# Kernel tuning notes

Hardware: AMD Instinct MI355X
Metric: run time of the kernel (lower is better)

The kernel has to match this reference:

```python
import jax, jax.numpy as jnp
import numpy as np

D = 1024      # n_embd
H = 16        # n_head
DH = D // H   # head dim = 64
FF = 4 * D    # 4096
EPS = 1e-5
MASKED_BIAS = -10000.0


def gelu_new(x):
    # GPT-2 'gelu_new': 0.5*x*(1+tanh(sqrt(2/pi)*(x+0.044715*x^3)))
    c = np.sqrt(2.0 / np.pi).astype(np.float32)
    return 0.5 * x * (1.0 + jnp.tanh(c * (x + 0.044715 * x * x * x)))


def layer_norm(x, g, b):
    mu = jnp.mean(x, axis=-1, keepdims=True)
    var = jnp.mean(jnp.square(x - mu), axis=-1, keepdims=True)
    return (x - mu) * jax.lax.rsqrt(var + EPS) * g + b


def setup_inputs() -> dict:
    key = jax.random.key(0)
    ks = jax.random.split(key, 8)
    B, S = 4, 2048
    std = 0.02
    return {
        "hidden_states": jax.random.normal(ks[0], (B, S, D), jnp.float32),
        "ln1_g": jnp.ones((D,), jnp.float32),
        "ln1_b": jnp.zeros((D,), jnp.float32),
        "w_attn": std * jax.random.normal(ks[1], (D, 3 * D), jnp.float32),
        "b_attn": jnp.zeros((3 * D,), jnp.float32),
        "w_attn_proj": std * jax.random.normal(ks[2], (D, D), jnp.float32),
        "b_attn_proj": jnp.zeros((D,), jnp.float32),
        "ln2_g": jnp.ones((D,), jnp.float32),
        "ln2_b": jnp.zeros((D,), jnp.float32),
        "w_fc": std * jax.random.normal(ks[3], (D, FF), jnp.float32),
        "b_fc": jnp.zeros((FF,), jnp.float32),
        "w_mlp_proj": std * jax.random.normal(ks[4], (FF, D), jnp.float32),
        "b_mlp_proj": jnp.zeros((D,), jnp.float32),
    }


def reference(hidden_states, ln1_g, ln1_b, w_attn, b_attn, w_attn_proj, b_attn_proj,
              ln2_g, ln2_b, w_fc, b_fc, w_mlp_proj, b_mlp_proj):
    B, S, _ = hidden_states.shape

    # --- self-attention ---
    x = layer_norm(hidden_states, ln1_g, ln1_b)
    qkv = x @ w_attn + b_attn                       # [B,S,3D]
    q, k, v = jnp.split(qkv, 3, axis=-1)
    # split heads -> [B,H,S,DH]
    q = q.reshape(B, S, H, DH).transpose(0, 2, 1, 3)
    k = k.reshape(B, S, H, DH).transpose(0, 2, 1, 3)
    v = v.reshape(B, S, H, DH).transpose(0, 2, 1, 3)

    w = jnp.einsum('bhqd,bhkd->bhqk', q, k) / jnp.sqrt(jnp.float32(DH))
    causal = jnp.tril(jnp.ones((S, S), bool))       # [S,S]
    w = jnp.where(causal, w, jnp.float32(MASKED_BIAS))
    w = jax.nn.softmax(w, axis=-1)
    a = jnp.einsum('bhqk,bhkd->bhqd', w, v)         # [B,H,S,DH]
    a = a.transpose(0, 2, 1, 3).reshape(B, S, D)
    a = a @ w_attn_proj + b_attn_proj
    hidden_states = hidden_states + a

    # --- MLP ---
    m = layer_norm(hidden_states, ln2_g, ln2_b)
    m = gelu_new(m @ w_fc + b_fc) @ w_mlp_proj + b_mlp_proj
    return hidden_states + m
```

## Files before the change

kernel.cpp:

```cpp
#include <hip/hip_runtime.h>
#include <hip/hip_bf16.h>
#include <cstddef>

#define SEQ   2048
#define DMODEL 1024
#define NHEAD 16
#define HDIM  64
#define FFDIM 4096

typedef __attribute__((ext_vector_type(8))) short bf16x8;
typedef __attribute__((ext_vector_type(4))) short bf16x4;
typedef __attribute__((ext_vector_type(4))) float f32x4;

__device__ __forceinline__ unsigned short f2b(float x) {
  __hip_bfloat16 h = __float2bfloat16(x);
  return __builtin_bit_cast(unsigned short, h);
}
__device__ __forceinline__ float b2f(short u) {
  unsigned x = ((unsigned)(unsigned short)u) << 16;
  return __builtin_bit_cast(float, x);
}
__device__ __forceinline__ void gl16(const short* g, short* l) {
  __builtin_amdgcn_global_load_lds(
      (const __attribute__((address_space(1))) void*)g,
      (__attribute__((address_space(3))) void*)l, 16, 0, 0);
}

__global__ __launch_bounds__(256)
void ln_kernel(const float* __restrict__ x, const float* __restrict__ g,
               const float* __restrict__ b, short* __restrict__ y) {
  const int row = blockIdx.x;
  const int t = threadIdx.x;
  const float* xr = x + (size_t)row * DMODEL;
  float4 v = *(const float4*)(xr + t * 4);
  float s = v.x + v.y + v.z + v.w;
  float q = v.x * v.x + v.y * v.y + v.z * v.z + v.w * v.w;
  #pragma unroll
  for (int off = 32; off; off >>= 1) {
    s += __shfl_xor(s, off);
    q += __shfl_xor(q, off);
  }
  __shared__ float ss[4], qq[4];
  if ((t & 63) == 0) { ss[t >> 6] = s; qq[t >> 6] = q; }
  __syncthreads();
  s = ss[0] + ss[1] + ss[2] + ss[3];
  q = qq[0] + qq[1] + qq[2] + qq[3];
  const float mean = s * (1.f / DMODEL);
  const float var = q * (1.f / DMODEL) - mean * mean;
  const float rstd = rsqrtf(var + 1e-5f);
  float4 gv = *(const float4*)(g + t * 4);
  float4 bv = *(const float4*)(b + t * 4);
  bf16x4 o;
  o[0] = (short)f2b((v.x - mean) * rstd * gv.x + bv.x);
  o[1] = (short)f2b((v.y - mean) * rstd * gv.y + bv.y);
  o[2] = (short)f2b((v.z - mean) * rstd * gv.z + bv.z);
  o[3] = (short)f2b((v.w - mean) * rstd * gv.w + bv.w);
  *(bf16x4*)(y + (size_t)row * DMODEL + t * 4) = o;
}

__device__ __forceinline__ float gelu_new_f(float x) {
  const float c = 0.7978845608028654f;
  float u = c * (x + 0.044715f * x * x * x);
  float e = __expf(2.f * u);
  float t = 1.f - 2.f / (e + 1.f);
  return 0.5f * x * (1.f + t);
}

__global__ __launch_bounds__(256)
void wconv_kernel(const float* __restrict__ W, short* __restrict__ Wt,
                  int K, int N) {
  const int n0 = blockIdx.x * 64, k0 = blockIdx.y * 64;
  const int t = threadIdx.x;
  __shared__ short tile[64][72];
  #pragma unroll
  for (int i = 0; i < 4; ++i) {
    const int row = i * 16 + (t >> 4);
    const int col4 = (t & 15) * 4;
    float4 v = *(const float4*)(W + (size_t)(k0 + row) * N + n0 + col4);
    tile[col4 + 0][row] = (short)f2b(v.x);
    tile[col4 + 1][row] = (short)f2b(v.y);
    tile[col4 + 2][row] = (short)f2b(v.z);
    tile[col4 + 3][row] = (short)f2b(v.w);
  }
  __syncthreads();
  #pragma unroll
  for (int i = 0; i < 2; ++i) {
    const int cc = t + i * 256;
    const int nr = cc >> 3, k8 = (cc & 7) * 8;
    bf16x8 vv;
    #pragma unroll
    for (int j = 0; j < 8; ++j) vv[j] = tile[nr][k8 + j];
    *(bf16x8*)(Wt + (size_t)(n0 + nr) * K + k0 + k8) = vv;
  }
}

template <bool OUTBF, bool GELU, bool RES>
__global__ __launch_bounds__(256)
void gemm_bf16(const short* __restrict__ A, const short* __restrict__ Bt,
               const float* __restrict__ bias, const float* __restrict__ R,
               void* __restrict__ C, int M, int N, int K) {
  __shared__ short As[128 * 64];
  __shared__ short Bs[128 * 64];
  const int t = threadIdx.x, lane = t & 63, w = t >> 6;
  const int g = lane >> 4, la = lane & 15;
  const int bn = blockIdx.x, bm = blockIdx.y;
  const int wm = w >> 1, wn = w & 1;

  const int srow = t >> 3;
  const int scolb = ((t & 7) * 16) ^ ((srow & 7) << 4);
  const short* Ag = A + (size_t)(bm * 128 + srow) * K + (scolb >> 1);
  const short* Bg = Bt + (size_t)(bn * 128 + srow) * K + (scolb >> 1);
  short* Asl = As + t * 8;
  short* Bsl = Bs + t * 8;

  f32x4 acc[4][4];
  #pragma unroll
  for (int i = 0; i < 4; ++i)
    #pragma unroll
    for (int j = 0; j < 4; ++j) acc[i][j] = (f32x4){0.f, 0.f, 0.f, 0.f};

  const int KT = K >> 6;
  for (int kt = 0; kt < KT; ++kt) {
    __syncthreads();
    #pragma unroll
    for (int i = 0; i < 4; ++i) {
      gl16(Ag + (size_t)i * 32 * K + kt * 64, Asl + i * 2048);
      gl16(Bg + (size_t)i * 32 * K + kt * 64, Bsl + i * 2048);
    }
    __syncthreads();
    #pragma unroll
    for (int ks = 0; ks < 2; ++ks) {
      bf16x8 af[4], bfr[4];
      #pragma unroll
      for (int mi = 0; mi < 4; ++mi) {
        const int row = wm * 64 + mi * 16 + la;
        af[mi] = *(const bf16x8*)((const char*)As + row * 128 +
                                  ((ks * 64 + g * 16) ^ ((row & 7) << 4)));
      }
      #pragma unroll
      for (int ni = 0; ni < 4; ++ni) {
        const int row = wn * 64 + ni * 16 + la;
        bfr[ni] = *(const bf16x8*)((const char*)Bs + row * 128 +
                                   ((ks * 64 + g * 16) ^ ((row & 7) << 4)));
      }
      #pragma unroll
      for (int mi = 0; mi < 4; ++mi)
        #pragma unroll
        for (int ni = 0; ni < 4; ++ni)
          acc[mi][ni] = __builtin_amdgcn_mfma_f32_16x16x32_bf16(
              af[mi], bfr[ni], acc[mi][ni], 0, 0, 0);
    }
  }

  const int crow0 = bm * 128 + wm * 64 + g * 4;
  const int ccol0 = bn * 128 + wn * 64 + la;
  float bl[4];
  #pragma unroll
  for (int ni = 0; ni < 4; ++ni) bl[ni] = bias[ccol0 + ni * 16];
  #pragma unroll
  for (int mi = 0; mi < 4; ++mi) {
    #pragma unroll
    for (int r = 0; r < 4; ++r) {
      const size_t row = (size_t)(crow0 + mi * 16 + r);
      #pragma unroll
      for (int ni = 0; ni < 4; ++ni) {
        float v = acc[mi][ni][r] + bl[ni];
        if (GELU) v = gelu_new_f(v);
        if (RES) v += R[row * N + ccol0 + ni * 16];
        if (OUTBF)
          ((short*)C)[row * N + ccol0 + ni * 16] = (short)f2b(v);
        else
          ((float*)C)[row * N + ccol0 + ni * 16] = v;
      }
    }
  }
}

__global__ __launch_bounds__(256)
void prep_kernel(const short* __restrict__ qkv, short* __restrict__ Qb,
                 short* __restrict__ Kb, short* __restrict__ Vtb) {
  const int st = blockIdx.x, h = blockIdx.y, b = blockIdx.z;
  const int t = threadIdx.x;
  const int s0 = st * 64;
  const size_t bh = (size_t)b * NHEAD + h;
  __shared__ short vt[64][72];
  #pragma unroll
  for (int i = 0; i < 2; ++i) {
    const int cc = t + i * 256;
    const int r = cc >> 3, d8 = (cc & 7) * 8;
    const short* src = qkv + ((size_t)b * SEQ + s0 + r) * 3072 + h * 64 + d8;
    bf16x8 q8 = *(const bf16x8*)(src);
    #pragma unroll
    for (int j = 0; j < 8; ++j) q8[j] = (short)f2b(b2f(q8[j]) * 0.125f);
    *(bf16x8*)(Qb + (bh * SEQ + s0 + r) * 64 + d8) = q8;
    bf16x8 k8 = *(const bf16x8*)(src + 1024);
    *(bf16x8*)(Kb + (bh * SEQ + s0 + r) * 64 + d8) = k8;
    bf16x8 v8 = *(const bf16x8*)(src + 2048);
    #pragma unroll
    for (int j = 0; j < 8; ++j) vt[d8 + j][r] = v8[j];
  }
  __syncthreads();
  #pragma unroll
  for (int i = 0; i < 2; ++i) {
    const int cc = t + i * 256;
    const int d = cc >> 3, s8 = (cc & 7) * 8;
    bf16x8 vv;
    #pragma unroll
    for (int j = 0; j < 8; ++j) vv[j] = vt[d][s8 + j];
    *(bf16x8*)(Vtb + (bh * 64 + d) * SEQ + s0 + s8) = vv;
  }
}

__global__ __launch_bounds__(256)
void mha_kernel(const short* __restrict__ Qb, const short* __restrict__ Kb,
                const short* __restrict__ Vtb, short* __restrict__ out) {
  const int qt = blockIdx.x, h = blockIdx.y, b = blockIdx.z;
  const int t = threadIdx.x, lane = t & 63, w = t >> 6;
  const int g = lane >> 4, la = lane & 15;
  const size_t bh = (size_t)b * NHEAD + h;

  __shared__ short Ks[64 * 64];
  __shared__ short Vts[64 * 64];
  __shared__ short Ps[4][16 * 64];

  const short* qrow = Qb + (bh * SEQ + (size_t)qt * 64 + w * 16 + la) * 64;
  const bf16x8 qf0 = *(const bf16x8*)(qrow + g * 8);
  const bf16x8 qf1 = *(const bf16x8*)(qrow + 32 + g * 8);

  float o[16];
  #pragma unroll
  for (int i = 0; i < 16; ++i) o[i] = 0.f;
  float m = -1e30f, l = 0.f;

  const int sr0 = t >> 3, sc8 = (t & 7) * 8;

  for (int kt = 0; kt <= qt; ++kt) {
    const int k0 = kt * 64;
    __syncthreads();
    #pragma unroll
    for (int i = 0; i < 2; ++i) {
      const int r = sr0 + i * 32;
      bf16x8 kv = *(const bf16x8*)(Kb + (bh * SEQ + k0 + r) * 64 + sc8);
      bf16x8 vv = *(const bf16x8*)(Vtb + (bh * 64 + r) * SEQ + k0 + sc8);
      const int lb = r * 128 + ((sc8 * 2) ^ ((r & 7) << 4));
      *(bf16x8*)((char*)Ks + lb) = kv;
      *(bf16x8*)((char*)Vts + lb) = vv;
    }
    __syncthreads();

    float sv[16];
    #pragma unroll
    for (int mt = 0; mt < 4; ++mt) {
      const int ar = mt * 16 + la;
      const int ab = ar * 128 + ((g * 16) ^ ((ar & 7) << 4));
      bf16x8 ka0 = *(const bf16x8*)((char*)Ks + ab);
      bf16x8 ka1 = *(const bf16x8*)((char*)Ks + (ab ^ 64));
      f32x4 sa = {0.f, 0.f, 0.f, 0.f};
      sa = __builtin_amdgcn_mfma_f32_16x16x32_bf16(ka0, qf0, sa, 0, 0, 0);
      sa = __builtin_amdgcn_mfma_f32_16x16x32_bf16(ka1, qf1, sa, 0, 0, 0);
      sv[mt * 4 + 0] = sa[0]; sv[mt * 4 + 1] = sa[1];
      sv[mt * 4 + 2] = sa[2]; sv[mt * 4 + 3] = sa[3];
    }

    if (kt == qt) {
      const int qrel = w * 16 + la;
      #pragma unroll
      for (int idx = 0; idx < 16; ++idx) {
        const int krel = (idx >> 2) * 16 + g * 4 + (idx & 3);
        if (krel > qrel) sv[idx] = -10000.0f;
      }
    }

    float tmax = sv[0];
    #pragma unroll
    for (int i = 1; i < 16; ++i) tmax = fmaxf(tmax, sv[i]);
    tmax = fmaxf(tmax, __shfl_xor(tmax, 16));
    tmax = fmaxf(tmax, __shfl_xor(tmax, 32));
    const float mn = fmaxf(m, tmax);
    const float sc = __expf(m - mn);
    m = mn;
    float ps = 0.f;
    #pragma unroll
    for (int i = 0; i < 16; ++i) { sv[i] = __expf(sv[i] - mn); ps += sv[i]; }
    ps += __shfl_xor(ps, 16);
    ps += __shfl_xor(ps, 32);
    l = l * sc + ps;
    #pragma unroll
    for (int r = 0; r < 4; ++r) {
      const float scr = __shfl(sc, (g << 2) + r);
      o[r] *= scr; o[4 + r] *= scr; o[8 + r] *= scr; o[12 + r] *= scr;
    }
    #pragma unroll
    for (int mt = 0; mt < 4; ++mt) {
      #pragma unroll
      for (int r2 = 0; r2 < 2; ++r2) {
        const unsigned pk = (unsigned)f2b(sv[mt * 4 + r2 * 2]) |
                            ((unsigned)f2b(sv[mt * 4 + r2 * 2 + 1]) << 16);
        const int kk = mt * 16 + g * 4 + r2 * 2;
        const int pb = la * 128 + ((kk * 2) ^ ((la & 7) << 4));
        *(unsigned*)((char*)Ps[w] + pb) = pk;
      }
    }
    asm volatile("s_waitcnt lgkmcnt(0)" ::: "memory");
    __builtin_amdgcn_sched_barrier(0);

    const int pb0 = la * 128 + ((g * 16) ^ ((la & 7) << 4));
    const bf16x8 pa0 = *(const bf16x8*)((char*)Ps[w] + pb0);
    const bf16x8 pa1 = *(const bf16x8*)((char*)Ps[w] + (pb0 ^ 64));
    #pragma unroll
    for (int nt = 0; nt < 4; ++nt) {
      const int dr = nt * 16 + la;
      const int vb = dr * 128 + ((g * 16) ^ ((dr & 7) << 4));
      bf16x8 vb0 = *(const bf16x8*)((char*)Vts + vb);
      bf16x8 vb1 = *(const bf16x8*)((char*)Vts + (vb ^ 64));
      f32x4 oa = {o[nt * 4 + 0], o[nt * 4 + 1], o[nt * 4 + 2], o[nt * 4 + 3]};
      oa = __builtin_amdgcn_mfma_f32_16x16x32_bf16(pa0, vb0, oa, 0, 0, 0);
      oa = __builtin_amdgcn_mfma_f32_16x16x32_bf16(pa1, vb1, oa, 0, 0, 0);
      o[nt * 4 + 0] = oa[0]; o[nt * 4 + 1] = oa[1];
      o[nt * 4 + 2] = oa[2]; o[nt * 4 + 3] = oa[3];
    }
  }

  const float linv = 1.f / l;
  #pragma unroll
  for (int r = 0; r < 4; ++r) {
    const float li = __shfl(linv, (g << 2) + r);
    const int qrow_g = qt * 64 + w * 16 + g * 4 + r;
    #pragma unroll
    for (int nt = 0; nt < 4; ++nt) {
      out[((size_t)b * SEQ + qrow_g) * DMODEL + h * 64 + nt * 16 + la] =
          (short)f2b(o[nt * 4 + r] * li);
    }
  }
}

extern "C" void kernel_launch(void* const* d_in, const int* in_sizes, int n_in,
                              void* d_out, int out_size, void* d_ws, size_t ws_size,
                              hipStream_t stream) {
  const float* hidden      = (const float*)d_in[0];
  const float* ln1_g       = (const float*)d_in[1];
  const float* ln1_b       = (const float*)d_in[2];
  const float* w_attn      = (const float*)d_in[3];
  const float* b_attn      = (const float*)d_in[4];
  const float* w_attn_proj = (const float*)d_in[5];
  const float* b_attn_proj = (const float*)d_in[6];
  const float* ln2_g       = (const float*)d_in[7];
  const float* ln2_b       = (const float*)d_in[8];
  const float* w_fc        = (const float*)d_in[9];
  const float* b_fc        = (const float*)d_in[10];
  const float* w_mlp_proj  = (const float*)d_in[11];
  const float* b_mlp_proj  = (const float*)d_in[12];
  float* out = (float*)d_out;

  const int Bn = in_sizes[0] / (SEQ * DMODEL);
  const int M = Bn * SEQ;

  char* W = (char*)d_ws;
  const size_t szMD2 = (size_t)M * DMODEL * 2;
  short* xln_b  = (short*)W;
  short* qkv_b  = (short*)(W + szMD2);
  short* a1_b   = qkv_b;
  char*  p2     = W + szMD2 + (size_t)M * FFDIM * 2;
  short* Qb     = (short*)p2;
  short* Kb     = Qb + (size_t)M * DMODEL;
  short* Vtb    = Kb + (size_t)M * DMODEL;
  short* attn_b = Vtb + (size_t)M * DMODEL;
  float* h2     = (float*)(p2 + 4 * szMD2);
  short* wat    = (short*)(p2 + 4 * szMD2 + (size_t)M * DMODEL * 4);
  short* wpt    = wat + (size_t)3 * DMODEL * DMODEL;
  short* wft    = wpt + (size_t)DMODEL * DMODEL;
  short* wmt    = wft + (size_t)FFDIM * DMODEL;

  wconv_kernel<<<dim3(3 * DMODEL / 64, DMODEL / 64), 256, 0, stream>>>(
      w_attn, wat, DMODEL, 3 * DMODEL);
  wconv_kernel<<<dim3(DMODEL / 64, DMODEL / 64), 256, 0, stream>>>(
      w_attn_proj, wpt, DMODEL, DMODEL);
  wconv_kernel<<<dim3(FFDIM / 64, DMODEL / 64), 256, 0, stream>>>(
      w_fc, wft, DMODEL, FFDIM);
  wconv_kernel<<<dim3(DMODEL / 64, FFDIM / 64), 256, 0, stream>>>(
      w_mlp_proj, wmt, FFDIM, DMODEL);

  ln_kernel<<<M, 256, 0, stream>>>(hidden, ln1_g, ln1_b, xln_b);
  gemm_bf16<true, false, false><<<dim3(3 * DMODEL / 128, M / 128), 256, 0, stream>>>(
      xln_b, wat, b_attn, nullptr, qkv_b, M, 3 * DMODEL, DMODEL);
  prep_kernel<<<dim3(SEQ / 64, NHEAD, Bn), 256, 0, stream>>>(qkv_b, Qb, Kb, Vtb);
  mha_kernel<<<dim3(SEQ / 64, NHEAD, Bn), 256, 0, stream>>>(Qb, Kb, Vtb, attn_b);
  gemm_bf16<false, false, true><<<dim3(DMODEL / 128, M / 128), 256, 0, stream>>>(
      attn_b, wpt, b_attn_proj, hidden, h2, M, DMODEL, DMODEL);
  ln_kernel<<<M, 256, 0, stream>>>(h2, ln2_g, ln2_b, xln_b);
  gemm_bf16<true, true, false><<<dim3(FFDIM / 128, M / 128), 256, 0, stream>>>(
      xln_b, wft, b_fc, nullptr, a1_b, M, FFDIM, DMODEL);
  gemm_bf16<false, false, true><<<dim3(DMODEL / 128, M / 128), 256, 0, stream>>>(
      a1_b, wmt, b_mlp_proj, h2, out, M, DMODEL, FFDIM);
}
```

Before: 618.6 us.

## Pair causal query tiles per block and streamline flash-attention softmax

The attention kernel now processes two query tiles per block (p and QT-1-p), so every block does about the same causal work, and it launches half as many blocks. Softmax switches to exp2, with log2(e) folded into the Q scale and the mask constant. A lazy rescale skips the output correction when the running max grows by little, and the max and sum reductions become trees. K/V tiles are loaded with direct global-to-LDS loads, and the four weight-conversion launches are merged into one. The lazy-rescale threshold lets unnormalized values grow up to 2^11.5 before correction, which carries a small numerical risk.

```diff
diff --git a/kernel.cpp b/kernel.cpp
--- a/kernel.cpp
+++ b/kernel.cpp
@@ -7,6 +7,7 @@
 #define NHEAD 16
 #define HDIM  64
 #define FFDIM 4096
+#define QT    (SEQ / 64)
 
 typedef __attribute__((ext_vector_type(8))) short bf16x8;
 typedef __attribute__((ext_vector_type(4))) short bf16x4;
@@ -67,9 +68,18 @@
 }
 
 __global__ __launch_bounds__(256)
-void wconv_kernel(const float* __restrict__ W, short* __restrict__ Wt,
-                  int K, int N) {
-  const int n0 = blockIdx.x * 64, k0 = blockIdx.y * 64;
+void wconv4_kernel(const float* __restrict__ w0, short* __restrict__ t0,
+                   const float* __restrict__ w1, short* __restrict__ t1,
+                   const float* __restrict__ w2, short* __restrict__ t2,
+                   const float* __restrict__ w3, short* __restrict__ t3) {
+  int id = blockIdx.x;
+  const float* W; short* Wt; int K, N;
+  if (id < 768)       { W = w0; Wt = t0; K = 1024; N = 3072; }
+  else if (id < 1024) { id -= 768;  W = w1; Wt = t1; K = 1024; N = 1024; }
+  else if (id < 2048) { id -= 1024; W = w2; Wt = t2; K = 1024; N = 4096; }
+  else                { id -= 2048; W = w3; Wt = t3; K = 4096; N = 1024; }
+  const int nt = N >> 6;
+  const int n0 = (id % nt) * 64, k0 = (id / nt) * 64;
   const int t = threadIdx.x;
   __shared__ short tile[64][72];
   #pragma unroll
@@ -183,6 +193,7 @@
   const int t = threadIdx.x;
   const int s0 = st * 64;
   const size_t bh = (size_t)b * NHEAD + h;
+  const float qscale = 0.125f * 1.44269504088896f;
   __shared__ short vt[64][72];
   #pragma unroll
   for (int i = 0; i < 2; ++i) {
@@ -191,7 +202,7 @@
     const short* src = qkv + ((size_t)b * SEQ + s0 + r) * 3072 + h * 64 + d8;
     bf16x8 q8 = *(const bf16x8*)(src);
     #pragma unroll
-    for (int j = 0; j < 8; ++j) q8[j] = (short)f2b(b2f(q8[j]) * 0.125f);
+    for (int j = 0; j < 8; ++j) q8[j] = (short)f2b(b2f(q8[j]) * qscale);
     *(bf16x8*)(Qb + (bh * SEQ + s0 + r) * 64 + d8) = q8;
     bf16x8 k8 = *(const bf16x8*)(src + 1024);
     *(bf16x8*)(Kb + (bh * SEQ + s0 + r) * 64 + d8) = k8;
@@ -214,7 +225,7 @@
 __global__ __launch_bounds__(256)
 void mha_kernel(const short* __restrict__ Qb, const short* __restrict__ Kb,
                 const short* __restrict__ Vtb, short* __restrict__ out) {
-  const int qt = blockIdx.x, h = blockIdx.y, b = blockIdx.z;
+  const int p = blockIdx.x, h = blockIdx.y, b = blockIdx.z;
   const int t = threadIdx.x, lane = t & 63, w = t >> 6;
   const int g = lane >> 4, la = lane & 15;
   const size_t bh = (size_t)b * NHEAD + h;
@@ -223,113 +234,134 @@
   __shared__ short Vts[64 * 64];
   __shared__ short Ps[4][16 * 64];
 
-  const short* qrow = Qb + (bh * SEQ + (size_t)qt * 64 + w * 16 + la) * 64;
-  const bf16x8 qf0 = *(const bf16x8*)(qrow + g * 8);
-  const bf16x8 qf1 = *(const bf16x8*)(qrow + 32 + g * 8);
-
-  float o[16];
-  #pragma unroll
-  for (int i = 0; i < 16; ++i) o[i] = 0.f;
-  float m = -1e30f, l = 0.f;
-
-  const int sr0 = t >> 3, sc8 = (t & 7) * 8;
-
-  for (int kt = 0; kt <= qt; ++kt) {
-    const int k0 = kt * 64;
-    __syncthreads();
-    #pragma unroll
-    for (int i = 0; i < 2; ++i) {
-      const int r = sr0 + i * 32;
-      bf16x8 kv = *(const bf16x8*)(Kb + (bh * SEQ + k0 + r) * 64 + sc8);
-      bf16x8 vv = *(const bf16x8*)(Vtb + (bh * 64 + r) * SEQ + k0 + sc8);
-      const int lb = r * 128 + ((sc8 * 2) ^ ((r & 7) << 4));
-      *(bf16x8*)((char*)Ks + lb) = kv;
-      *(bf16x8*)((char*)Vts + lb) = vv;
+  const int srow = t >> 3;
+  const int scolb = ((t & 7) * 16) ^ ((srow & 7) << 4);
+
+  #pragma unroll 1
+  for (int e = 0; e < 2; ++e) {
+    const int qt = e ? (QT - 1 - p) : p;
+
+    const short* qrow = Qb + (bh * SEQ + (size_t)qt * 64 + w * 16 + la) * 64;
+    const bf16x8 qf0 = *(const bf16x8*)(qrow + g * 8);
+    const bf16x8 qf1 = *(const bf16x8*)(qrow + 32 + g * 8);
+
+    float o[16];
+    #pragma unroll
+    for (int i = 0; i < 16; ++i) o[i] = 0.f;
+    float m = -1e30f, l = 0.f;
+
+    for (int kt = 0; kt <= qt; ++kt) {
+      const int k0 = kt * 64;
+      __syncthreads();
+      #pragma unroll
+      for (int i = 0; i < 2; ++i) {
+        const int r = srow + i * 32;
+        gl16(Kb + (bh * SEQ + k0 + r) * 64 + (scolb >> 1), Ks + i * 2048 + t * 8);
+        gl16(Vtb + (bh * 64 + r) * SEQ + k0 + (scolb >> 1), Vts + i * 2048 + t * 8);
+      }
+      __syncthreads();
+
+      float sv[16];
+      #pragma unroll
+      for (int mt = 0; mt < 4; ++mt) {
+        const int ar = mt * 16 + la;
+        const int ab = ar * 128 + ((g * 16) ^ ((ar & 7) << 4));
+        bf16x8 ka0 = *(const bf16x8*)((char*)Ks + ab);
+        bf16x8 ka1 = *(const bf16x8*)((char*)Ks + (ab ^ 64));
+        f32x4 sa = {0.f, 0.f, 0.f, 0.f};
+        sa = __builtin_amdgcn_mfma_f32_16x16x32_bf16(ka0, qf0, sa, 0, 0, 0);
+        sa = __builtin_amdgcn_mfma_f32_16x16x32_bf16(ka1, qf1, sa, 0, 0, 0);
+        sv[mt * 4 + 0] = sa[0]; sv[mt * 4 + 1] = sa[1];
+        sv[mt * 4 + 2] = sa[2]; sv[mt * 4 + 3] = sa[3];
+      }
+
+      if (kt == qt) {
+        const int qrel = w * 16 + la;
+        #pragma unroll
+        for (int idx = 0; idx < 16; ++idx) {
+          const int krel = (idx >> 2) * 16 + g * 4 + (idx & 3);
+          if (krel > qrel) sv[idx] = -14426.950408889634f;
+        }
+      }
+
+      float t8[8], t4[4], t2[2];
+      #pragma unroll
+      for (int i = 0; i < 8; ++i) t8[i] = fmaxf(sv[2 * i], sv[2 * i + 1]);
+      #pragma unroll
+      for (int i = 0; i < 4; ++i) t4[i] = fmaxf(t8[2 * i], t8[2 * i + 1]);
+      t2[0] = fmaxf(t4[0], t4[1]); t2[1] = fmaxf(t4[2], t4[3]);
+      float tmax = fmaxf(t2[0], t2[1]);
+      tmax = fmaxf(tmax, __shfl_xor(tmax, 16));
+      tmax = fmaxf(tmax, __shfl_xor(tmax, 32));
+
+      const bool skip = __all(tmax <= m + 11.5f) != 0;
+      const float mn = skip ? m : fmaxf(m, tmax);
+
+      float ss8[8], ss4[4];
+      #pragma unroll
+      for (int i = 0; i < 16; ++i) sv[i] = exp2f(sv[i] - mn);
+      #pragma unroll
+      for (int i = 0; i < 8; ++i) ss8[i] = sv[2 * i] + sv[2 * i + 1];
+      #pragma unroll
+      for (int i = 0; i < 4; ++i) ss4[i] = ss8[2 * i] + ss8[2 * i + 1];
+      float ps = (ss4[0] + ss4[1]) + (ss4[2] + ss4[3]);
+      ps += __shfl_xor(ps, 16);
+      ps += __shfl_xor(ps, 32);
+
+      if (skip) {
+        l += ps;
+      } else {
+        const float sc = exp2f(m - mn);
+        l = l * sc + ps;
+        m = mn;
+        #pragma unroll
+        for (int r = 0; r < 4; ++r) {
+          const float scr = __shfl(sc, (g << 2) + r);
+          o[r] *= scr; o[4 + r] *= scr; o[8 + r] *= scr; o[12 + r] *= scr;
+        }
+      }
+
+      #pragma unroll
+      for (int mt = 0; mt < 4; ++mt) {
+        #pragma unroll
+        for (int r2 = 0; r2 < 2; ++r2) {
+          const unsigned pk = (unsigned)f2b(sv[mt * 4 + r2 * 2]) |
+                              ((unsigned)f2b(sv[mt * 4 + r2 * 2 + 1]) << 16);
+          const int kk = mt * 16 + g * 4 + r2 * 2;
+          const int pb = la * 128 + ((kk * 2) ^ ((la & 7) << 4));
+          *(unsigned*)((char*)Ps[w] + pb) = pk;
+        }
+      }
+      asm volatile("s_waitcnt lgkmcnt(0)" ::: "memory");
+      __builtin_amdgcn_sched_barrier(0);
+
+      const int pb0 = la * 128 + ((g * 16) ^ ((la & 7) << 4));
+      const bf16x8 pa0 = *(const bf16x8*)((char*)Ps[w] + pb0);
+      const bf16x8 pa1 = *(const bf16x8*)((char*)Ps[w] + (pb0 ^ 64));
+      #pragma unroll
+      for (int nt = 0; nt < 4; ++nt) {
+        const int dr = nt * 16 + la;
+        const int vb = dr * 128 + ((g * 16) ^ ((dr & 7) << 4));
+        bf16x8 vb0 = *(const bf16x8*)((char*)Vts + vb);
+        bf16x8 vb1 = *(const bf16x8*)((char*)Vts + (vb ^ 64));
+        f32x4 oa = {o[nt * 4 + 0], o[nt * 4 + 1], o[nt * 4 + 2], o[nt * 4 + 3]};
+        oa = __builtin_amdgcn_mfma_f32_16x16x32_bf16(pa0, vb0, oa, 0, 0, 0);
+        oa = __builtin_amdgcn_mfma_f32_16x16x32_bf16(pa1, vb1, oa, 0, 0, 0);
+        o[nt * 4 + 0] = oa[0]; o[nt * 4 + 1] = oa[1];
+        o[nt * 4 + 2] = oa[2]; o[nt * 4 + 3] = oa[3];
+      }
     }
-    __syncthreads();
-
-    float sv[16];
-    #pragma unroll
-    for (int mt = 0; mt < 4; ++mt) {
-      const int ar = mt * 16 + la;
-      const int ab = ar * 128 + ((g * 16) ^ ((ar & 7) << 4));
-      bf16x8 ka0 = *(const bf16x8*)((char*)Ks + ab);
-      bf16x8 ka1 = *(const bf16x8*)((char*)Ks + (ab ^ 64));
-      f32x4 sa = {0.f, 0.f, 0.f, 0.f};
-      sa = __builtin_amdgcn_mfma_f32_16x16x32_bf16(ka0, qf0, sa, 0, 0, 0);
-      sa = __builtin_amdgcn_mfma_f32_16x16x32_bf16(ka1, qf1, sa, 0, 0, 0);
-      sv[mt * 4 + 0] = sa[0]; sv[mt * 4 + 1] = sa[1];
-      sv[mt * 4 + 2] = sa[2]; sv[mt * 4 + 3] = sa[3];
-    }
-
-    if (kt == qt) {
-      const int qrel = w * 16 + la;
-      #pragma unroll
-      for (int idx = 0; idx < 16; ++idx) {
-        const int krel = (idx >> 2) * 16 + g * 4 + (idx & 3);
-        if (krel > qrel) sv[idx] = -10000.0f;
-      }
-    }
-
-    float tmax = sv[0];
-    #pragma unroll
-    for (int i = 1; i < 16; ++i) tmax = fmaxf(tmax, sv[i]);
-    tmax = fmaxf(tmax, __shfl_xor(tmax, 16));
-    tmax = fmaxf(tmax, __shfl_xor(tmax, 32));
-    const float mn = fmaxf(m, tmax);
-    const float sc = __expf(m - mn);
-    m = mn;
-    float ps = 0.f;
-    #pragma unroll
-    for (int i = 0; i < 16; ++i) { sv[i] = __expf(sv[i] - mn); ps += sv[i]; }
-    ps += __shfl_xor(ps, 16);
-    ps += __shfl_xor(ps, 32);
-    l = l * sc + ps;
+
+    const float linv = 1.f / l;
     #pragma unroll
     for (int r = 0; r < 4; ++r) {
-      const float scr = __shfl(sc, (g << 2) + r);
-      o[r] *= scr; o[4 + r] *= scr; o[8 + r] *= scr; o[12 + r] *= scr;
-    }
-    #pragma unroll
-    for (int mt = 0; mt < 4; ++mt) {
-      #pragma unroll
-      for (int r2 = 0; r2 < 2; ++r2) {
-        const unsigned pk = (unsigned)f2b(sv[mt * 4 + r2 * 2]) |
-                            ((unsigned)f2b(sv[mt * 4 + r2 * 2 + 1]) << 16);
-        const int kk = mt * 16 + g * 4 + r2 * 2;
-        const int pb = la * 128 + ((kk * 2) ^ ((la & 7) << 4));
-        *(unsigned*)((char*)Ps[w] + pb) = pk;
-      }
-    }
-    asm volatile("s_waitcnt lgkmcnt(0)" ::: "memory");
-    __builtin_amdgcn_sched_barrier(0);
-
-    const int pb0 = la * 128 + ((g * 16) ^ ((la & 7) << 4));
-    const bf16x8 pa0 = *(const bf16x8*)((char*)Ps[w] + pb0);
-    const bf16x8 pa1 = *(const bf16x8*)((char*)Ps[w] + (pb0 ^ 64));
-    #pragma unroll
-    for (int nt = 0; nt < 4; ++nt) {
-      const int dr = nt * 16 + la;
-      const int vb = dr * 128 + ((g * 16) ^ ((dr & 7) << 4));
-      bf16x8 vb0 = *(const bf16x8*)((char*)Vts + vb);
-      bf16x8 vb1 = *(const bf16x8*)((char*)Vts + (vb ^ 64));
-      f32x4 oa = {o[nt * 4 + 0], o[nt * 4 + 1], o[nt * 4 + 2], o[nt * 4 + 3]};
-      oa = __builtin_amdgcn_mfma_f32_16x16x32_bf16(pa0, vb0, oa, 0, 0, 0);
-      oa = __builtin_amdgcn_mfma_f32_16x16x32_bf16(pa1, vb1, oa, 0, 0, 0);
-      o[nt * 4 + 0] = oa[0]; o[nt * 4 + 1] = oa[1];
-      o[nt * 4 + 2] = oa[2]; o[nt * 4 + 3] = oa[3];
-    }
-  }
-
-  const float linv = 1.f / l;
-  #pragma unroll
-  for (int r = 0; r < 4; ++r) {
-    const float li = __shfl(linv, (g << 2) + r);
-    const int qrow_g = qt * 64 + w * 16 + g * 4 + r;
-    #pragma unroll
-    for (int nt = 0; nt < 4; ++nt) {
-      out[((size_t)b * SEQ + qrow_g) * DMODEL + h * 64 + nt * 16 + la] =
-          (short)f2b(o[nt * 4 + r] * li);
+      const float li = __shfl(linv, (g << 2) + r);
+      const int qrow_g = qt * 64 + w * 16 + g * 4 + r;
+      #pragma unroll
+      for (int nt = 0; nt < 4; ++nt) {
+        out[((size_t)b * SEQ + qrow_g) * DMODEL + h * 64 + nt * 16 + la] =
+            (short)f2b(o[nt * 4 + r] * li);
+      }
     }
   }
 }
@@ -371,20 +403,13 @@
   short* wft    = wpt + (size_t)DMODEL * DMODEL;
   short* wmt    = wft + (size_t)FFDIM * DMODEL;
 
-  wconv_kernel<<<dim3(3 * DMODEL / 64, DMODEL / 64), 256, 0, stream>>>(
-      w_attn, wat, DMODEL, 3 * DMODEL);
-  wconv_kernel<<<dim3(DMODEL / 64, DMODEL / 64), 256, 0, stream>>>(
-      w_attn_proj, wpt, DMODEL, DMODEL);
-  wconv_kernel<<<dim3(FFDIM / 64, DMODEL / 64), 256, 0, stream>>>(
-      w_fc, wft, DMODEL, FFDIM);
-  wconv_kernel<<<dim3(DMODEL / 64, FFDIM / 64), 256, 0, stream>>>(
-      w_mlp_proj, wmt, FFDIM, DMODEL);
-
+  wconv4_kernel<<<3072, 256, 0, stream>>>(w_attn, wat, w_attn_proj, wpt,
+                                          w_fc, wft, w_mlp_proj, wmt);
   ln_kernel<<<M, 256, 0, stream>>>(hidden, ln1_g, ln1_b, xln_b);
   gemm_bf16<true, false, false><<<dim3(3 * DMODEL / 128, M / 128), 256, 0, stream>>>(
       xln_b, wat, b_attn, nullptr, qkv_b, M, 3 * DMODEL, DMODEL);
   prep_kernel<<<dim3(SEQ / 64, NHEAD, Bn), 256, 0, stream>>>(qkv_b, Qb, Kb, Vtb);
-  mha_kernel<<<dim3(SEQ / 64, NHEAD, Bn), 256, 0, stream>>>(Qb, Kb, Vtb, attn_b);
+  mha_kernel<<<dim3(QT / 2, NHEAD, Bn), 256, 0, stream>>>(Qb, Kb, Vtb, attn_b);
   gemm_bf16<false, false, true><<<dim3(DMODEL / 128, M / 128), 256, 0, stream>>>(
       attn_b, wpt, b_attn_proj, hidden, h2, M, DMODEL, DMODEL);
   ln_kernel<<<M, 256, 0, stream>>>(h2, ln2_g, ln2_b, xln_b);
```

New measurement: 565.3 us. 1.09x faster.
